# Optimization experiments

Measured on AMD Instinct MI355X. Metric: run time of the kernel, lower is better.

The kernel has to match this reference:

```python
import jax, jax.numpy as jnp
import numpy as np

N = 500000
M = 8  # max vertices after clipping a 4-gon by 4 half-planes


def _angle_sort(q):
    # q: (4,2) points in convex position -> CCW-ordered convex quad (== convex hull)
    c = q.mean(axis=0)
    ang = jnp.arctan2(q[:, 1] - c[1], q[:, 0] - c[0])
    return q[jnp.argsort(ang)]


def _poly_inter_area(subj, clip):
    # Sutherland-Hodgman clipping of CCW convex quad `subj` by CCW convex quad `clip`.
    poly = jnp.zeros((M, 2), subj.dtype).at[:4].set(subj)
    n = jnp.array(4, jnp.int32)
    edges = jnp.stack([clip, jnp.roll(clip, -1, axis=0)], axis=1)  # (4,2,2)

    def clip_edge(state, edge):
        poly, n = state
        a, b = edge[0], edge[1]
        e = b - a
        idx = jnp.arange(M)
        n_safe = jnp.maximum(n, 1)
        nxt = poly[(idx + 1) % n_safe]
        d_cur = e[0] * (poly[:, 1] - a[1]) - e[1] * (poly[:, 0] - a[0])
        d_nxt = e[0] * (nxt[:, 1] - a[1]) - e[1] * (nxt[:, 0] - a[0])
        in_cur = d_cur >= 0
        in_nxt = d_nxt >= 0
        den = d_cur - d_nxt
        den = jnp.where(jnp.abs(den) < 1e-12, 1e-12, den)
        t = (d_cur / den)[:, None]
        ipt = poly + t * (nxt - poly)
        active = idx < n
        pts = jnp.stack([poly, ipt], axis=1).reshape(2 * M, 2)
        valid = jnp.stack([active & in_cur, active & (in_cur != in_nxt)], axis=1).reshape(2 * M)
        pos = jnp.cumsum(valid) - 1
        new_poly = jnp.zeros((M, 2), poly.dtype).at[jnp.where(valid, pos, M)].set(pts, mode='drop')
        return (new_poly, jnp.sum(valid).astype(jnp.int32)), None

    (poly, n), _ = jax.lax.scan(clip_edge, (poly, n), edges)
    idx = jnp.arange(M)
    n_safe = jnp.maximum(n, 1)
    nxtv = poly[(idx + 1) % n_safe]
    mask = (idx < n).astype(poly.dtype)
    return 0.5 * jnp.abs(jnp.sum(mask * (poly[:, 0] * nxtv[:, 1] - nxtv[:, 0] * poly[:, 1])))


def _hull_area8(pts):
    # Area of convex hull of 8 points via gift wrapping (fixed 8 steps, pads by repeating start).
    P = 8
    start = jnp.argmin(pts[:, 1]).astype(jnp.int32)

    def next_idx(cur):
        rel = pts - pts[cur]
        d2 = jnp.sum(rel * rel, axis=1)
        C = rel[:, 0, None] * rel[None, :, 1] - rel[:, 1, None] * rel[None, :, 0]  # C[j,k]=cross(rel_j, rel_k)
        valid = jnp.all(C >= -1e-6, axis=1) & (d2 > 1e-12)  # all points left of cur->j
        score = jnp.where(valid, d2, -1.0)
        return jnp.argmax(score).astype(jnp.int32)

    def step(carry, _):
        cur, done = carry
        nxt = next_idx(cur)
        nxt = jnp.where(done, cur, nxt)
        done = done | (nxt == start)
        return (nxt, done), nxt

    _, seq = jax.lax.scan(step, (start, jnp.array(False)), None, length=P)
    order = jnp.concatenate([start[None], seq])  # (9,)
    v = pts[order]
    x, y = v[:, 0], v[:, 1]
    xn, yn = jnp.roll(x, -1), jnp.roll(y, -1)
    return 0.5 * jnp.abs(jnp.sum(x * yn - xn * y))


def _pair_loss(pred8, tgt8):
    p = _angle_sort(pred8.reshape(4, 2))
    t = _angle_sort(tgt8.reshape(4, 2))
    inter = _poly_inter_area(p, t)
    hull = _hull_area8(jnp.concatenate([p, t], axis=0))  # convex hull of union of points
    iou = jnp.where(hull > 1e-12, inter / jnp.maximum(hull, 1e-12), 0.0)
    return 1.0 - iou  # reduction='none', loss_type='iou'


def setup_inputs() -> dict:
    key = jax.random.key(0)
    ks = jax.random.split(key, 6)

    def make_quads(ka, kb, kc):
        # 4 vertices in convex position: sorted angles + radius in [0.5, 1.5]
        ang = jnp.sort(jax.random.uniform(ka, (N, 4)) * (2.0 * np.pi), axis=1)
        rad = 0.5 + jax.random.uniform(kb, (N, 4))
        ctr = jax.random.normal(kc, (N, 1, 2)) * 0.5
        pts = ctr + jnp.stack([rad * jnp.cos(ang), rad * jnp.sin(ang)], axis=-1)
        return pts.reshape(N, 8).astype(jnp.float32)

    preds = make_quads(ks[0], ks[1], ks[2])
    targets = make_quads(ks[3], ks[4], ks[5])
    return {"preds": preds, "targets": targets}


def reference(preds, targets):
    return jax.vmap(_pair_loss)(preds, targets)
```

## Files before the change

kernel.cpp:

```cpp
#include <hip/hip_runtime.h>
#include <math.h>

struct V2 { float x, y; };

#define NT 128

__device__ __forceinline__ int ang_class(float x, float y) {
    return (y < 0.f) ? 0 : ((y > 0.f) ? 2 : ((x >= 0.f) ? 1 : 3));
}

__device__ __forceinline__ void angle_sort4(float4 lo, float4 hi, V2 out[4]) {
    float x[4] = {lo.x, lo.z, hi.x, hi.z};
    float y[4] = {lo.y, lo.w, hi.y, hi.w};
    float cx = (((x[0] + x[1]) + x[2]) + x[3]) * 0.25f;
    float cy = (((y[0] + y[1]) + y[2]) + y[3]) * 0.25f;
    float rx[4], ry[4]; int cl[4];
#pragma unroll
    for (int i = 0; i < 4; i++) {
        rx[i] = x[i] - cx; ry[i] = y[i] - cy;
        cl[i] = ang_class(rx[i], ry[i]);
    }
#define CE(i, j) { \
    int cd = cl[i] - cl[j]; \
    double cr = (double)rx[i] * (double)ry[j] - (double)ry[i] * (double)rx[j]; \
    bool gt = (cd > 0) || (cd == 0 && cr < 0.0);   \
    float t; int ti; \
    t = x[i];  x[i]  = gt ? x[j]  : x[i];  x[j]  = gt ? t  : x[j]; \
    t = y[i];  y[i]  = gt ? y[j]  : y[i];  y[j]  = gt ? t  : y[j]; \
    t = rx[i]; rx[i] = gt ? rx[j] : rx[i]; rx[j] = gt ? t  : rx[j]; \
    t = ry[i]; ry[i] = gt ? ry[j] : ry[i]; ry[j] = gt ? t  : ry[j]; \
    ti = cl[i]; cl[i] = gt ? cl[j] : cl[i]; cl[j] = gt ? ti : cl[j]; \
}
    CE(0, 1) CE(2, 3) CE(0, 2) CE(1, 3) CE(1, 2)
#undef CE
#pragma unroll
    for (int k = 0; k < 4; k++) { out[k].x = x[k]; out[k].y = y[k]; }
}

__device__ __forceinline__ int clip_mid(float2 (*buf)[NT], V2 A, V2 B,
                                        int nv, int tid)
{
    float ex = B.x - A.x, ey = B.y - A.y;
    float qx[8], qy[8], d[8];
#pragma unroll
    for (int s = 0; s < 8; s++) {
        float2 v = buf[s][tid];
        qx[s] = v.x; qy[s] = v.y;
        d[s] = ex * (v.y - A.y) - ey * (v.x - A.x);
    }
    int cnt = 0;
#pragma unroll
    for (int idx = 0; idx < 8; idx++) {
        float nxx, nxy, dn;
        if (idx == 7) {
            bool w = (nv == 8);
            nxx = w ? qx[0] : qx[7];
            nxy = w ? qy[0] : qy[7];
            dn  = w ? d[0]  : d[7];
        } else {
            bool w = ((idx + 1) == nv);
            nxx = w ? qx[0] : qx[idx + 1];
            nxy = w ? qy[0] : qy[idx + 1];
            dn  = w ? d[0]  : d[idx + 1];
        }
        bool active = idx < nv;
        bool in_cur = d[idx] >= 0.f;
        bool in_nxt = dn >= 0.f;
        float den = d[idx] - dn;
        den = (fabsf(den) < 1e-12f) ? 1e-12f : den;
        float t = __fdividef(d[idx], den);
        float ix = qx[idx] + t * (nxx - qx[idx]);
        float iy = qy[idx] + t * (nxy - qy[idx]);
        bool v0 = active && in_cur;
        bool v1 = active && (in_cur != in_nxt);
        int s0 = (v0 && cnt < 8) ? cnt : 8;
        buf[s0][tid] = make_float2(qx[idx], qy[idx]);
        cnt += v0 ? 1 : 0;
        int s1 = (v1 && cnt < 8) ? cnt : 8;
        buf[s1][tid] = make_float2(ix, iy);
        cnt += v1 ? 1 : 0;
    }
    return cnt;
}

__device__ __forceinline__ float clip_final(const float2 (*buf)[NT], V2 A, V2 B,
                                            int nv, int tid)
{
    float ex = B.x - A.x, ey = B.y - A.y;
    float qx[8], qy[8], d[8];
#pragma unroll
    for (int s = 0; s < 8; s++) {
        float2 v = buf[s][tid];
        qx[s] = v.x; qy[s] = v.y;
        d[s] = ex * (v.y - A.y) - ey * (v.x - A.x);
    }
    int cnt = 0;
    float sx = 0.f;
    float fx = 0.f, fy = 0.f;
    float px = 0.f, py = 0.f;
#pragma unroll
    for (int idx = 0; idx < 8; idx++) {
        float nxx, nxy, dn;
        if (idx == 7) {
            bool w = (nv == 8);
            nxx = w ? qx[0] : qx[7];
            nxy = w ? qy[0] : qy[7];
            dn  = w ? d[0]  : d[7];
        } else {
            bool w = ((idx + 1) == nv);
            nxx = w ? qx[0] : qx[idx + 1];
            nxy = w ? qy[0] : qy[idx + 1];
            dn  = w ? d[0]  : d[idx + 1];
        }
        bool active = idx < nv;
        bool in_cur = d[idx] >= 0.f;
        bool in_nxt = dn >= 0.f;
        float den = d[idx] - dn;
        den = (fabsf(den) < 1e-12f) ? 1e-12f : den;
        float t = __fdividef(d[idx], den);
        float ix = qx[idx] + t * (nxx - qx[idx]);
        float iy = qy[idx] + t * (nxy - qy[idx]);
        bool v0 = active && in_cur;
        bool v1 = active && (in_cur != in_nxt);
        {
            bool w0 = (cnt == 0), wl = (cnt <= 7);
            if (v0) {
                fx = w0 ? qx[idx] : fx; fy = w0 ? qy[idx] : fy;
                sx += (!w0 && wl) ? (px * qy[idx] - qx[idx] * py) : 0.f;
                px = wl ? qx[idx] : px; py = wl ? qy[idx] : py;
            }
            cnt += v0 ? 1 : 0;
        }
        {
            bool w0 = (cnt == 0), wl = (cnt <= 7);
            if (v1) {
                fx = w0 ? ix : fx; fy = w0 ? iy : fy;
                sx += (!w0 && wl) ? (px * iy - ix * py) : 0.f;
                px = wl ? ix : px; py = wl ? iy : py;
            }
            cnt += v1 ? 1 : 0;
        }
    }
    if (cnt > 0 && cnt <= 8) sx += px * fy - fx * py;
    return 0.5f * fabsf(sx);
}

__global__ __launch_bounds__(NT, 8) void poly_iou_kernel(
    const float* __restrict__ preds, const float* __restrict__ targets,
    float* __restrict__ out, int n)
{
    __shared__ float2 buf[9][NT];
    int tid = threadIdx.x;
    int gid = blockIdx.x * NT + tid;
    if (gid >= n) return;

    const float4* p4 = reinterpret_cast<const float4*>(preds);
    const float4* t4 = reinterpret_cast<const float4*>(targets);
    float4 a0 = p4[2 * gid], a1 = p4[2 * gid + 1];
    float4 b0 = t4[2 * gid], b1 = t4[2 * gid + 1];

    V2 P[4], T[4];
    angle_sort4(a0, a1, P);
    angle_sort4(b0, b1, T);

    int nv;
    {
        float ex = T[1].x - T[0].x, ey = T[1].y - T[0].y;
        float dd[4];
#pragma unroll
        for (int k = 0; k < 4; k++)
            dd[k] = ex * (P[k].y - T[0].y) - ey * (P[k].x - T[0].x);
        int cnt = 0;
#pragma unroll
        for (int idx = 0; idx < 4; idx++) {
            int j = (idx + 1) & 3;
            bool in_cur = dd[idx] >= 0.f;
            bool in_nxt = dd[j] >= 0.f;
            float den = dd[idx] - dd[j];
            den = (fabsf(den) < 1e-12f) ? 1e-12f : den;
            float t = __fdividef(dd[idx], den);
            float ix = P[idx].x + t * (P[j].x - P[idx].x);
            float iy = P[idx].y + t * (P[j].y - P[idx].y);
            bool v1 = (in_cur != in_nxt);
            int s0 = in_cur ? cnt : 8;
            buf[s0][tid] = make_float2(P[idx].x, P[idx].y);
            cnt += in_cur ? 1 : 0;
            int s1 = v1 ? cnt : 8;
            buf[s1][tid] = make_float2(ix, iy);
            cnt += v1 ? 1 : 0;
        }
        nv = cnt;
    }

    nv = clip_mid(buf, T[1], T[2], nv, tid);
    nv = clip_mid(buf, T[2], T[3], nv, tid);
    float inter = clip_final(buf, T[3], T[0], nv, tid);

    V2 h[8];
#pragma unroll
    for (int k = 0; k < 4; k++) { h[k] = P[k]; h[4 + k] = T[k]; }

    int start = 0; V2 vs = h[0];
#pragma unroll
    for (int k = 1; k < 8; k++) {
        bool b = h[k].y < vs.y;
        start = b ? k : start;
        vs.x  = b ? h[k].x : vs.x;
        vs.y  = b ? h[k].y : vs.y;
    }

    V2 pc = vs; int cur = start; bool done = false; float harea = 0.f;
#pragma unroll 1
    for (int s = 0; s < 8; s++) {
        int best = cur;
        float bx = 0.f, by = 0.f, bd = 0.f, px = pc.x, py = pc.y;
#pragma unroll
        for (int k = 0; k < 8; k++) {
            float rx = h[k].x - pc.x, ry = h[k].y - pc.y;
            float d2 = rx * rx + ry * ry;
            bool ok = d2 > 1e-12f;
            float c = bx * ry - by * rx;
            bool take = ok && ((c < 0.f) || ((c == 0.f) && (d2 > bd)));
            best = take ? k : best;
            bx = take ? rx : bx; by = take ? ry : by; bd = take ? d2 : bd;
            px = take ? h[k].x : px; py = take ? h[k].y : py;
        }
        int nxt = done ? cur : best;
        V2 pv;
        pv.x = done ? pc.x : px;
        pv.y = done ? pc.y : py;
        harea += pc.x * pv.y - pv.x * pc.y;
        done = done || (nxt == start);
        pc = pv; cur = nxt;
        if (__all(done)) break;
    }
    harea += pc.x * vs.y - vs.x * pc.y;
    harea = 0.5f * fabsf(harea);

    float iou = (harea > 1e-12f) ? (inter / fmaxf(harea, 1e-12f)) : 0.f;
    out[gid] = 1.f - iou;
}

extern "C" void kernel_launch(void* const* d_in, const int* in_sizes, int n_in,
                              void* d_out, int out_size, void* d_ws, size_t ws_size,
                              hipStream_t stream) {
    const float* preds = (const float*)d_in[0];
    const float* targets = (const float*)d_in[1];
    float* out = (float*)d_out;
    int n = in_sizes[0] / 8;
    int block = NT;
    int grid = (n + block - 1) / block;
    hipLaunchKernelGGL(poly_iou_kernel, dim3(grid), dim3(block), 0, stream,
                       preds, targets, out, n);
}
```

Measured before the change: 33.59 us.

## Process two polygon pairs per thread with interleaved clipping and hull loops

Each thread now handles two independent pred/target pairs, with the two sets of clipping and gift-wrapping computations interleaved to raise instruction-level parallelism. The shared buffer grows to 256 slots per block, the grid is halved, and launch bounds drop from 8 to 4 waves per SIMD to leave room for the extra registers. The cost is higher register pressure and lower occupancy. The hull loop now exits only when both pairs in every lane are done, so more iterations may run.

```diff
diff --git a/kernel.cpp b/kernel.cpp
--- a/kernel.cpp
+++ b/kernel.cpp
@@ -4,6 +4,7 @@
 struct V2 { float x, y; };
 
 #define NT 128
+#define PPB (2 * NT)
 
 __device__ __forceinline__ int ang_class(float x, float y) {
     return (y < 0.f) ? 0 : ((y > 0.f) ? 2 : ((x >= 0.f) ? 1 : 3));
@@ -37,139 +38,170 @@
     for (int k = 0; k < 4; k++) { out[k].x = x[k]; out[k].y = y[k]; }
 }
 
-__device__ __forceinline__ int clip_mid(float2 (*buf)[NT], V2 A, V2 B,
-                                        int nv, int tid)
+__device__ __forceinline__ void clip_mid2(float2 (*buf)[PPB],
+                                          const V2* A, const V2* B,
+                                          int* nv, int tid)
 {
-    float ex = B.x - A.x, ey = B.y - A.y;
-    float qx[8], qy[8], d[8];
-#pragma unroll
-    for (int s = 0; s < 8; s++) {
-        float2 v = buf[s][tid];
-        qx[s] = v.x; qy[s] = v.y;
-        d[s] = ex * (v.y - A.y) - ey * (v.x - A.x);
-    }
-    int cnt = 0;
+    float ex[2], ey[2], qx[2][8], qy[2][8], d[2][8];
+#pragma unroll
+    for (int p = 0; p < 2; p++) {
+        ex[p] = B[p].x - A[p].x; ey[p] = B[p].y - A[p].y;
+#pragma unroll
+        for (int s = 0; s < 8; s++) {
+            float2 v = buf[s][tid + p * NT];
+            qx[p][s] = v.x; qy[p][s] = v.y;
+            d[p][s] = ex[p] * (v.y - A[p].y) - ey[p] * (v.x - A[p].x);
+        }
+    }
+    int cnt[2] = {0, 0};
 #pragma unroll
     for (int idx = 0; idx < 8; idx++) {
-        float nxx, nxy, dn;
-        if (idx == 7) {
-            bool w = (nv == 8);
-            nxx = w ? qx[0] : qx[7];
-            nxy = w ? qy[0] : qy[7];
-            dn  = w ? d[0]  : d[7];
-        } else {
-            bool w = ((idx + 1) == nv);
-            nxx = w ? qx[0] : qx[idx + 1];
-            nxy = w ? qy[0] : qy[idx + 1];
-            dn  = w ? d[0]  : d[idx + 1];
-        }
-        bool active = idx < nv;
-        bool in_cur = d[idx] >= 0.f;
-        bool in_nxt = dn >= 0.f;
-        float den = d[idx] - dn;
-        den = (fabsf(den) < 1e-12f) ? 1e-12f : den;
-        float t = __fdividef(d[idx], den);
-        float ix = qx[idx] + t * (nxx - qx[idx]);
-        float iy = qy[idx] + t * (nxy - qy[idx]);
-        bool v0 = active && in_cur;
-        bool v1 = active && (in_cur != in_nxt);
-        int s0 = (v0 && cnt < 8) ? cnt : 8;
-        buf[s0][tid] = make_float2(qx[idx], qy[idx]);
-        cnt += v0 ? 1 : 0;
-        int s1 = (v1 && cnt < 8) ? cnt : 8;
-        buf[s1][tid] = make_float2(ix, iy);
-        cnt += v1 ? 1 : 0;
-    }
-    return cnt;
-}
-
-__device__ __forceinline__ float clip_final(const float2 (*buf)[NT], V2 A, V2 B,
-                                            int nv, int tid)
+#pragma unroll
+        for (int p = 0; p < 2; p++) {
+            float nxx, nxy, dn;
+            if (idx == 7) {
+                bool w = (nv[p] == 8);
+                nxx = w ? qx[p][0] : qx[p][7];
+                nxy = w ? qy[p][0] : qy[p][7];
+                dn  = w ? d[p][0]  : d[p][7];
+            } else {
+                bool w = ((idx + 1) == nv[p]);
+                nxx = w ? qx[p][0] : qx[p][idx + 1];
+                nxy = w ? qy[p][0] : qy[p][idx + 1];
+                dn  = w ? d[p][0]  : d[p][idx + 1];
+            }
+            bool active = idx < nv[p];
+            bool in_cur = d[p][idx] >= 0.f;
+            bool in_nxt = dn >= 0.f;
+            float den = d[p][idx] - dn;
+            den = (fabsf(den) < 1e-12f) ? 1e-12f : den;
+            float t = __fdividef(d[p][idx], den);
+            float ix = qx[p][idx] + t * (nxx - qx[p][idx]);
+            float iy = qy[p][idx] + t * (nxy - qy[p][idx]);
+            bool v0 = active && in_cur;
+            bool v1 = active && (in_cur != in_nxt);
+            int s0 = (v0 && cnt[p] < 8) ? cnt[p] : 8;
+            buf[s0][tid + p * NT] = make_float2(qx[p][idx], qy[p][idx]);
+            cnt[p] += v0 ? 1 : 0;
+            int s1 = (v1 && cnt[p] < 8) ? cnt[p] : 8;
+            buf[s1][tid + p * NT] = make_float2(ix, iy);
+            cnt[p] += v1 ? 1 : 0;
+        }
+    }
+    nv[0] = cnt[0]; nv[1] = cnt[1];
+}
+
+__device__ __forceinline__ void clip_final2(const float2 (*buf)[PPB],
+                                            const V2* A, const V2* B,
+                                            const int* nv, int tid,
+                                            float* inter)
 {
-    float ex = B.x - A.x, ey = B.y - A.y;
-    float qx[8], qy[8], d[8];
-#pragma unroll
-    for (int s = 0; s < 8; s++) {
-        float2 v = buf[s][tid];
-        qx[s] = v.x; qy[s] = v.y;
-        d[s] = ex * (v.y - A.y) - ey * (v.x - A.x);
-    }
-    int cnt = 0;
-    float sx = 0.f;
-    float fx = 0.f, fy = 0.f;
-    float px = 0.f, py = 0.f;
+    float ex[2], ey[2], qx[2][8], qy[2][8], d[2][8];
+#pragma unroll
+    for (int p = 0; p < 2; p++) {
+        ex[p] = B[p].x - A[p].x; ey[p] = B[p].y - A[p].y;
+#pragma unroll
+        for (int s = 0; s < 8; s++) {
+            float2 v = buf[s][tid + p * NT];
+            qx[p][s] = v.x; qy[p][s] = v.y;
+            d[p][s] = ex[p] * (v.y - A[p].y) - ey[p] * (v.x - A[p].x);
+        }
+    }
+    int cnt[2] = {0, 0};
+    float sx[2] = {0.f, 0.f};
+    float fx[2] = {0.f, 0.f}, fy[2] = {0.f, 0.f};
+    float px[2] = {0.f, 0.f}, py[2] = {0.f, 0.f};
 #pragma unroll
     for (int idx = 0; idx < 8; idx++) {
-        float nxx, nxy, dn;
-        if (idx == 7) {
-            bool w = (nv == 8);
-            nxx = w ? qx[0] : qx[7];
-            nxy = w ? qy[0] : qy[7];
-            dn  = w ? d[0]  : d[7];
-        } else {
-            bool w = ((idx + 1) == nv);
-            nxx = w ? qx[0] : qx[idx + 1];
-            nxy = w ? qy[0] : qy[idx + 1];
-            dn  = w ? d[0]  : d[idx + 1];
-        }
-        bool active = idx < nv;
-        bool in_cur = d[idx] >= 0.f;
-        bool in_nxt = dn >= 0.f;
-        float den = d[idx] - dn;
-        den = (fabsf(den) < 1e-12f) ? 1e-12f : den;
-        float t = __fdividef(d[idx], den);
-        float ix = qx[idx] + t * (nxx - qx[idx]);
-        float iy = qy[idx] + t * (nxy - qy[idx]);
-        bool v0 = active && in_cur;
-        bool v1 = active && (in_cur != in_nxt);
-        {
-            bool w0 = (cnt == 0), wl = (cnt <= 7);
-            if (v0) {
-                fx = w0 ? qx[idx] : fx; fy = w0 ? qy[idx] : fy;
-                sx += (!w0 && wl) ? (px * qy[idx] - qx[idx] * py) : 0.f;
-                px = wl ? qx[idx] : px; py = wl ? qy[idx] : py;
-            }
-            cnt += v0 ? 1 : 0;
-        }
-        {
-            bool w0 = (cnt == 0), wl = (cnt <= 7);
-            if (v1) {
-                fx = w0 ? ix : fx; fy = w0 ? iy : fy;
-                sx += (!w0 && wl) ? (px * iy - ix * py) : 0.f;
-                px = wl ? ix : px; py = wl ? iy : py;
-            }
-            cnt += v1 ? 1 : 0;
-        }
-    }
-    if (cnt > 0 && cnt <= 8) sx += px * fy - fx * py;
-    return 0.5f * fabsf(sx);
-}
-
-__global__ __launch_bounds__(NT, 8) void poly_iou_kernel(
+#pragma unroll
+        for (int p = 0; p < 2; p++) {
+            float nxx, nxy, dn;
+            if (idx == 7) {
+                bool w = (nv[p] == 8);
+                nxx = w ? qx[p][0] : qx[p][7];
+                nxy = w ? qy[p][0] : qy[p][7];
+                dn  = w ? d[p][0]  : d[p][7];
+            } else {
+                bool w = ((idx + 1) == nv[p]);
+                nxx = w ? qx[p][0] : qx[p][idx + 1];
+                nxy = w ? qy[p][0] : qy[p][idx + 1];
+                dn  = w ? d[p][0]  : d[p][idx + 1];
+            }
+            bool active = idx < nv[p];
+            bool in_cur = d[p][idx] >= 0.f;
+            bool in_nxt = dn >= 0.f;
+            float den = d[p][idx] - dn;
+            den = (fabsf(den) < 1e-12f) ? 1e-12f : den;
+            float t = __fdividef(d[p][idx], den);
+            float ix = qx[p][idx] + t * (nxx - qx[p][idx]);
+            float iy = qy[p][idx] + t * (nxy - qy[p][idx]);
+            bool v0 = active && in_cur;
+            bool v1 = active && (in_cur != in_nxt);
+            {
+                bool w0 = (cnt[p] == 0), wl = (cnt[p] <= 7);
+                if (v0) {
+                    fx[p] = w0 ? qx[p][idx] : fx[p];
+                    fy[p] = w0 ? qy[p][idx] : fy[p];
+                    sx[p] += (!w0 && wl) ? (px[p] * qy[p][idx] - qx[p][idx] * py[p]) : 0.f;
+                    px[p] = wl ? qx[p][idx] : px[p];
+                    py[p] = wl ? qy[p][idx] : py[p];
+                }
+                cnt[p] += v0 ? 1 : 0;
+            }
+            {
+                bool w0 = (cnt[p] == 0), wl = (cnt[p] <= 7);
+                if (v1) {
+                    fx[p] = w0 ? ix : fx[p];
+                    fy[p] = w0 ? iy : fy[p];
+                    sx[p] += (!w0 && wl) ? (px[p] * iy - ix * py[p]) : 0.f;
+                    px[p] = wl ? ix : px[p];
+                    py[p] = wl ? iy : py[p];
+                }
+                cnt[p] += v1 ? 1 : 0;
+            }
+        }
+    }
+#pragma unroll
+    for (int p = 0; p < 2; p++) {
+        if (cnt[p] > 0 && cnt[p] <= 8) sx[p] += px[p] * fy[p] - fx[p] * py[p];
+        inter[p] = 0.5f * fabsf(sx[p]);
+    }
+}
+
+__global__ __launch_bounds__(NT, 4) void poly_iou_kernel(
     const float* __restrict__ preds, const float* __restrict__ targets,
     float* __restrict__ out, int n)
 {
-    __shared__ float2 buf[9][NT];
+    __shared__ float2 buf[9][PPB];
     int tid = threadIdx.x;
-    int gid = blockIdx.x * NT + tid;
-    if (gid >= n) return;
+    int gid0 = blockIdx.x * PPB + tid;
+    int gid1 = gid0 + NT;
+    int g0 = min(gid0, n - 1);
+    int g1 = min(gid1, n - 1);
 
     const float4* p4 = reinterpret_cast<const float4*>(preds);
     const float4* t4 = reinterpret_cast<const float4*>(targets);
-    float4 a0 = p4[2 * gid], a1 = p4[2 * gid + 1];
-    float4 b0 = t4[2 * gid], b1 = t4[2 * gid + 1];
-
-    V2 P[4], T[4];
-    angle_sort4(a0, a1, P);
-    angle_sort4(b0, b1, T);
-
-    int nv;
+
+    V2 P[2][4], T[2][4];
     {
-        float ex = T[1].x - T[0].x, ey = T[1].y - T[0].y;
+        float4 a0 = p4[2 * g0], a1 = p4[2 * g0 + 1];
+        float4 b0 = t4[2 * g0], b1 = t4[2 * g0 + 1];
+        float4 a2 = p4[2 * g1], a3 = p4[2 * g1 + 1];
+        float4 b2 = t4[2 * g1], b3 = t4[2 * g1 + 1];
+        angle_sort4(a0, a1, P[0]);
+        angle_sort4(b0, b1, T[0]);
+        angle_sort4(a2, a3, P[1]);
+        angle_sort4(b2, b3, T[1]);
+    }
+
+    int nv[2];
+#pragma unroll
+    for (int p = 0; p < 2; p++) {
+        float ex = T[p][1].x - T[p][0].x, ey = T[p][1].y - T[p][0].y;
         float dd[4];
 #pragma unroll
         for (int k = 0; k < 4; k++)
-            dd[k] = ex * (P[k].y - T[0].y) - ey * (P[k].x - T[0].x);
+            dd[k] = ex * (P[p][k].y - T[p][0].y) - ey * (P[p][k].x - T[p][0].x);
         int cnt = 0;
 #pragma unroll
         for (int idx = 0; idx < 4; idx++) {
@@ -179,66 +211,95 @@
             float den = dd[idx] - dd[j];
             den = (fabsf(den) < 1e-12f) ? 1e-12f : den;
             float t = __fdividef(dd[idx], den);
-            float ix = P[idx].x + t * (P[j].x - P[idx].x);
-            float iy = P[idx].y + t * (P[j].y - P[idx].y);
+            float ix = P[p][idx].x + t * (P[p][j].x - P[p][idx].x);
+            float iy = P[p][idx].y + t * (P[p][j].y - P[p][idx].y);
             bool v1 = (in_cur != in_nxt);
             int s0 = in_cur ? cnt : 8;
-            buf[s0][tid] = make_float2(P[idx].x, P[idx].y);
+            buf[s0][tid + p * NT] = make_float2(P[p][idx].x, P[p][idx].y);
             cnt += in_cur ? 1 : 0;
             int s1 = v1 ? cnt : 8;
-            buf[s1][tid] = make_float2(ix, iy);
+            buf[s1][tid + p * NT] = make_float2(ix, iy);
             cnt += v1 ? 1 : 0;
         }
-        nv = cnt;
-    }
-
-    nv = clip_mid(buf, T[1], T[2], nv, tid);
-    nv = clip_mid(buf, T[2], T[3], nv, tid);
-    float inter = clip_final(buf, T[3], T[0], nv, tid);
-
-    V2 h[8];
-#pragma unroll
-    for (int k = 0; k < 4; k++) { h[k] = P[k]; h[4 + k] = T[k]; }
-
-    int start = 0; V2 vs = h[0];
-#pragma unroll
-    for (int k = 1; k < 8; k++) {
-        bool b = h[k].y < vs.y;
-        start = b ? k : start;
-        vs.x  = b ? h[k].x : vs.x;
-        vs.y  = b ? h[k].y : vs.y;
-    }
-
-    V2 pc = vs; int cur = start; bool done = false; float harea = 0.f;
+        nv[p] = cnt;
+    }
+
+    V2 A[2], B[2];
+    A[0] = T[0][1]; B[0] = T[0][2]; A[1] = T[1][1]; B[1] = T[1][2];
+    clip_mid2(buf, A, B, nv, tid);
+    A[0] = T[0][2]; B[0] = T[0][3]; A[1] = T[1][2]; B[1] = T[1][3];
+    clip_mid2(buf, A, B, nv, tid);
+    A[0] = T[0][3]; B[0] = T[0][0]; A[1] = T[1][3]; B[1] = T[1][0];
+    float inter[2];
+    clip_final2(buf, A, B, nv, tid, inter);
+
+    float hx[2][8], hy[2][8];
+#pragma unroll
+    for (int p = 0; p < 2; p++) {
+#pragma unroll
+        for (int k = 0; k < 4; k++) {
+            hx[p][k] = P[p][k].x;     hy[p][k] = P[p][k].y;
+            hx[p][4 + k] = T[p][k].x; hy[p][4 + k] = T[p][k].y;
+        }
+    }
+
+    int start[2]; float vsx[2], vsy[2];
+#pragma unroll
+    for (int p = 0; p < 2; p++) {
+        start[p] = 0; vsx[p] = hx[p][0]; vsy[p] = hy[p][0];
+#pragma unroll
+        for (int k = 1; k < 8; k++) {
+            bool b = hy[p][k] < vsy[p];
+            start[p] = b ? k : start[p];
+            vsx[p] = b ? hx[p][k] : vsx[p];
+            vsy[p] = b ? hy[p][k] : vsy[p];
+        }
+    }
+
+    float pcx[2], pcy[2], harea[2];
+    int cur[2]; bool done[2];
+#pragma unroll
+    for (int p = 0; p < 2; p++) {
+        pcx[p] = vsx[p]; pcy[p] = vsy[p];
+        cur[p] = start[p]; done[p] = false; harea[p] = 0.f;
+    }
 #pragma unroll 1
     for (int s = 0; s < 8; s++) {
-        int best = cur;
-        float bx = 0.f, by = 0.f, bd = 0.f, px = pc.x, py = pc.y;
-#pragma unroll
-        for (int k = 0; k < 8; k++) {
-            float rx = h[k].x - pc.x, ry = h[k].y - pc.y;
-            float d2 = rx * rx + ry * ry;
-            bool ok = d2 > 1e-12f;
-            float c = bx * ry - by * rx;
-            bool take = ok && ((c < 0.f) || ((c == 0.f) && (d2 > bd)));
-            best = take ? k : best;
-            bx = take ? rx : bx; by = take ? ry : by; bd = take ? d2 : bd;
-            px = take ? h[k].x : px; py = take ? h[k].y : py;
-        }
-        int nxt = done ? cur : best;
-        V2 pv;
-        pv.x = done ? pc.x : px;
-        pv.y = done ? pc.y : py;
-        harea += pc.x * pv.y - pv.x * pc.y;
-        done = done || (nxt == start);
-        pc = pv; cur = nxt;
-        if (__all(done)) break;
-    }
-    harea += pc.x * vs.y - vs.x * pc.y;
-    harea = 0.5f * fabsf(harea);
-
-    float iou = (harea > 1e-12f) ? (inter / fmaxf(harea, 1e-12f)) : 0.f;
-    out[gid] = 1.f - iou;
+#pragma unroll
+        for (int p = 0; p < 2; p++) {
+            int best = cur[p];
+            float bx = 0.f, by = 0.f, bd = 0.f, px = pcx[p], py = pcy[p];
+#pragma unroll
+            for (int k = 0; k < 8; k++) {
+                float rx = hx[p][k] - pcx[p], ry = hy[p][k] - pcy[p];
+                float d2 = rx * rx + ry * ry;
+                bool ok = d2 > 1e-12f;
+                float c = bx * ry - by * rx;
+                bool take = ok && ((c < 0.f) || ((c == 0.f) && (d2 > bd)));
+                best = take ? k : best;
+                bx = take ? rx : bx; by = take ? ry : by; bd = take ? d2 : bd;
+                px = take ? hx[p][k] : px; py = take ? hy[p][k] : py;
+            }
+            int nxt = done[p] ? cur[p] : best;
+            float pvx = done[p] ? pcx[p] : px;
+            float pvy = done[p] ? pcy[p] : py;
+            harea[p] += pcx[p] * pvy - pvx * pcy[p];
+            done[p] = done[p] || (nxt == start[p]);
+            pcx[p] = pvx; pcy[p] = pvy; cur[p] = nxt;
+        }
+        if (__all(done[0] && done[1])) break;
+    }
+
+#pragma unroll
+    for (int p = 0; p < 2; p++) {
+        harea[p] += pcx[p] * vsy[p] - vsx[p] * pcy[p];
+        harea[p] = 0.5f * fabsf(harea[p]);
+    }
+
+    float iou0 = (harea[0] > 1e-12f) ? (inter[0] / fmaxf(harea[0], 1e-12f)) : 0.f;
+    float iou1 = (harea[1] > 1e-12f) ? (inter[1] / fmaxf(harea[1], 1e-12f)) : 0.f;
+    if (gid0 < n) out[gid0] = 1.f - iou0;
+    if (gid1 < n) out[gid1] = 1.f - iou1;
 }
 
 extern "C" void kernel_launch(void* const* d_in, const int* in_sizes, int n_in,
@@ -248,8 +309,7 @@
     const float* targets = (const float*)d_in[1];
     float* out = (float*)d_out;
     int n = in_sizes[0] / 8;
-    int block = NT;
-    int grid = (n + block - 1) / block;
-    hipLaunchKernelGGL(poly_iou_kernel, dim3(grid), dim3(block), 0, stream,
+    int grid = (n + PPB - 1) / PPB;
+    hipLaunchKernelGGL(poly_iou_kernel, dim3(grid), dim3(NT), 0, stream,
                        preds, targets, out, n);
 }
```

After: 39.43 us. 17.4% more time.
